# Kernel optimization log

Measured on AMD Instinct MI355X. Metric: run time of the kernel, lower is better.

The kernel has to match this reference:

```python
import jax, jax.numpy as jnp
import numpy as np

N, T, D, H = 64, 1024, 512, 512

def setup_inputs() -> dict:
    key = jax.random.key(0)
    k1, k2, k3, k4 = jax.random.split(key, 4)
    x = jax.random.normal(k1, (N, T, D), dtype=jnp.float32)
    h0 = jax.random.normal(k2, (N, H), dtype=jnp.float32)
    Wx = jax.random.normal(k3, (D, H), dtype=jnp.float32) / jnp.sqrt(jnp.float32(D))
    Wh = jax.random.normal(k4, (H, H), dtype=jnp.float32) / jnp.sqrt(jnp.float32(H))
    b = jnp.zeros((H,), dtype=jnp.float32)
    return {"x": x, "h0": h0, "Wx": Wx, "Wh": Wh, "b": b}

def reference(x, h0, Wx, Wh, b):
    # Precompute input projection for all timesteps: (N,T,H)
    xW = jnp.einsum('ntd,dh->nth', x, Wx) + b
    # Sequential recurrence over time via lax.scan
    def step(prev_h, xw_t):
        next_h = jnp.tanh(prev_h @ Wh + xw_t)  # (N,H)
        return next_h, next_h
    # scan over time axis: move T to leading axis
    _, h_seq = jax.lax.scan(step, h0, jnp.swapaxes(xW, 0, 1))  # (T,N,H)
    return jnp.swapaxes(h_seq, 0, 1)  # (N,T,H)
```

## Files before the change

kernel.cpp:

```cpp
#include <hip/hip_runtime.h>
#include <hip/hip_fp16.h>
#include <cstddef>
#include <cstdint>

#define NB 64
#define TT 1024
#define DD 512
#define HH 512

typedef _Float16 h2_t __attribute__((ext_vector_type(2)));
typedef __attribute__((ext_vector_type(8))) short bf16x8;
typedef __attribute__((ext_vector_type(4))) float f32x4;
typedef __attribute__((ext_vector_type(8))) unsigned short ushort8;

__device__ __forceinline__ float dot2f(uint32_t a, uint32_t b, float c) {
#if __has_builtin(__builtin_amdgcn_fdot2)
    return __builtin_amdgcn_fdot2(__builtin_bit_cast(h2_t, a),
                                  __builtin_bit_cast(h2_t, b), c, false);
#else
    __half2 av = __builtin_bit_cast(__half2, a);
    __half2 bv = __builtin_bit_cast(__half2, b);
    float2 af = __half22float2(av), bf = __half22float2(bv);
    return fmaf(af.x, bf.x, fmaf(af.y, bf.y, c));
#endif
}

__device__ __forceinline__ float fast_tanh(float z) {
    z = fmaxf(-15.f, fminf(15.f, z));
    float u = __builtin_amdgcn_exp2f(-2.885390082f * z);
    return (1.f - u) * __builtin_amdgcn_rcpf(1.f + u);
}

__device__ __forceinline__ unsigned short f2bf(float f) {
    uint32_t u = __builtin_bit_cast(uint32_t, f);
    u += 0x7FFFu + ((u >> 16) & 1u);
    return (unsigned short)(u >> 16);
}

__global__ void conv_x(const float* __restrict__ x,
                       unsigned short* __restrict__ xb, long total) {
    long i0 = (long)(blockIdx.x * blockDim.x + threadIdx.x) * 8;
    long stride = (long)gridDim.x * blockDim.x * 8;
    for (long i = i0; i < total; i += stride) {
        float4 a = *reinterpret_cast<const float4*>(&x[i]);
        float4 b = *reinterpret_cast<const float4*>(&x[i + 4]);
        ushort8 o;
        o[0] = f2bf(a.x); o[1] = f2bf(a.y); o[2] = f2bf(a.z); o[3] = f2bf(a.w);
        o[4] = f2bf(b.x); o[5] = f2bf(b.y); o[6] = f2bf(b.z); o[7] = f2bf(b.w);
        *reinterpret_cast<ushort8*>(&xb[i]) = o;
    }
}

__global__ void conv_wt(const float* __restrict__ W,
                        unsigned short* __restrict__ Wt) {
    int n = blockIdx.x;
    int kc = threadIdx.x;
    ushort8 o;
#pragma unroll
    for (int i = 0; i < 8; ++i)
        o[i] = f2bf(W[(size_t)(kc * 8 + i) * HH + n]);
    *reinterpret_cast<ushort8*>(&Wt[(size_t)n * DD + kc * 8]) = o;
}

#define GBM 128
#define GBN 128
#define GBK 64
#define LDSW 72

__global__ __launch_bounds__(256, 4) void gemm_bf16(
    const unsigned short* __restrict__ A,
    const unsigned short* __restrict__ Bt,
    const float* __restrict__ bias,
    float* __restrict__ C)
{
    __shared__ unsigned short As[GBM * LDSW];
    __shared__ unsigned short Bs[GBN * LDSW];

    const int tid  = threadIdx.x;
    const int m0   = blockIdx.x * GBM;
    const int n0   = blockIdx.y * GBN;
    const int lane = tid & 63;
    const int wave = tid >> 6;
    const int wm   = wave >> 1;
    const int wn   = wave & 1;

    const int srow = tid >> 3;
    const int sch  = tid & 7;

    f32x4 acc[4][4] = {};

    const int arow = wm * 64 + (lane & 15);
    const int brow = wn * 64 + (lane & 15);
    const int koff = (lane >> 4) * 8;

    for (int kt = 0; kt < DD / GBK; ++kt) {
        const int k0 = kt * GBK;
#pragma unroll
        for (int p = 0; p < 4; ++p) {
            const int row = srow + p * 32;
            *reinterpret_cast<ushort8*>(&As[row * LDSW + sch * 8]) =
                *reinterpret_cast<const ushort8*>(
                    &A[(size_t)(m0 + row) * DD + k0 + sch * 8]);
            *reinterpret_cast<ushort8*>(&Bs[row * LDSW + sch * 8]) =
                *reinterpret_cast<const ushort8*>(
                    &Bt[(size_t)(n0 + row) * DD + k0 + sch * 8]);
        }
        __syncthreads();

#pragma unroll
        for (int kk = 0; kk < GBK; kk += 32) {
            bf16x8 af[4], bf[4];
#pragma unroll
            for (int mt = 0; mt < 4; ++mt)
                af[mt] = *reinterpret_cast<const bf16x8*>(
                    &As[(arow + mt * 16) * LDSW + kk + koff]);
#pragma unroll
            for (int nt = 0; nt < 4; ++nt)
                bf[nt] = *reinterpret_cast<const bf16x8*>(
                    &Bs[(brow + nt * 16) * LDSW + kk + koff]);
#pragma unroll
            for (int mt = 0; mt < 4; ++mt)
#pragma unroll
                for (int nt = 0; nt < 4; ++nt)
                    acc[mt][nt] = __builtin_amdgcn_mfma_f32_16x16x32_bf16(
                        af[mt], bf[nt], acc[mt][nt], 0, 0, 0);
        }
        __syncthreads();
    }

#pragma unroll
    for (int nt = 0; nt < 4; ++nt) {
        const int col = n0 + wn * 64 + nt * 16 + (lane & 15);
        const float bv = bias[col];
#pragma unroll
        for (int mt = 0; mt < 4; ++mt) {
            const int rbase = m0 + wm * 64 + mt * 16 + (lane >> 4) * 4;
#pragma unroll
            for (int r = 0; r < 4; ++r)
                C[(size_t)(rbase + r) * HH + col] = acc[mt][nt][r] + bv;
        }
    }
}

#define BM 128
#define BN 128
#define BK 8

__global__ __launch_bounds__(256, 2) void gemm_xw(
    const float* __restrict__ A,
    const float* __restrict__ B,
    const float* __restrict__ bias,
    float* __restrict__ C)
{
    __shared__ float As[BK][BM];
    __shared__ float Bs[BK][BN];

    const int tid  = threadIdx.x;
    const int tm   = tid >> 4;
    const int tn   = tid & 15;
    const int row0 = blockIdx.x * BM;
    const int col0 = blockIdx.y * BN;

    const int ar = tid >> 1;
    const int ac = (tid & 1) * 4;
    const int br = tid >> 5;
    const int bc = (tid & 31) * 4;

    float acc[8][8];
#pragma unroll
    for (int i = 0; i < 8; ++i)
#pragma unroll
        for (int j = 0; j < 8; ++j) acc[i][j] = 0.f;

    for (int k0 = 0; k0 < DD; k0 += BK) {
        float4 av = *reinterpret_cast<const float4*>(
            &A[(size_t)(row0 + ar) * DD + k0 + ac]);
        float4 bv = *reinterpret_cast<const float4*>(
            &B[(size_t)(k0 + br) * HH + col0 + bc]);

        As[ac + 0][ar] = av.x;
        As[ac + 1][ar] = av.y;
        As[ac + 2][ar] = av.z;
        As[ac + 3][ar] = av.w;
        *reinterpret_cast<float4*>(&Bs[br][bc]) = bv;
        __syncthreads();

#pragma unroll
        for (int kk = 0; kk < BK; ++kk) {
            float a[8], b[8];
            *reinterpret_cast<float4*>(&a[0]) =
                *reinterpret_cast<const float4*>(&As[kk][tm * 8]);
            *reinterpret_cast<float4*>(&a[4]) =
                *reinterpret_cast<const float4*>(&As[kk][tm * 8 + 4]);
            *reinterpret_cast<float4*>(&b[0]) =
                *reinterpret_cast<const float4*>(&Bs[kk][tn * 8]);
            *reinterpret_cast<float4*>(&b[4]) =
                *reinterpret_cast<const float4*>(&Bs[kk][tn * 8 + 4]);
#pragma unroll
            for (int i = 0; i < 8; ++i)
#pragma unroll
                for (int j = 0; j < 8; ++j)
                    acc[i][j] = fmaf(a[i], b[j], acc[i][j]);
        }
        __syncthreads();
    }

#pragma unroll
    for (int i = 0; i < 8; ++i) {
        const int row = row0 + tm * 8 + i;
#pragma unroll
        for (int j = 0; j < 8; j += 4) {
            const int col = col0 + tn * 8 + j;
            float4 o;
            o.x = acc[i][j + 0] + bias[col + 0];
            o.y = acc[i][j + 1] + bias[col + 1];
            o.z = acc[i][j + 2] + bias[col + 2];
            o.w = acc[i][j + 3] + bias[col + 3];
            *reinterpret_cast<float4*>(&C[(size_t)row * HH + col]) = o;
        }
    }
}

__global__ __launch_bounds__(1024, 4) void rnn_scan_pkt(
    const float* __restrict__ Wh,
    const float* __restrict__ h0,
    float* __restrict__ out,
    uint64_t* __restrict__ exch)
{
    __shared__ __align__(16) uint32_t hp[2][HH / 2];
    __shared__ float partial[16][128];

    const int blk = blockIdx.x;
    const int x = blk & 7;
    const int i = blk >> 3;
    const int n = x + ((i & 7) << 3);
    const int r = i >> 3;
    const int jb = r << 7;

    const int tid = threadIdx.x;
    const int w = tid >> 6;
    const int l = tid & 63;

    uint32_t w0[16], w1[16];
    {
        const float* wc = Wh + (size_t)(w * 32) * HH + jb + l;
#pragma unroll
        for (int p = 0; p < 16; ++p) {
            float e0 = wc[(size_t)(2 * p) * HH];
            float e1 = wc[(size_t)(2 * p + 1) * HH];
            w0[p] = __builtin_bit_cast(uint32_t, __floats2half2_rn(e0, e1));
            float f0 = wc[(size_t)(2 * p) * HH + 64];
            float f1 = wc[(size_t)(2 * p + 1) * HH + 64];
            w1[p] = __builtin_bit_cast(uint32_t, __floats2half2_rn(f0, f1));
        }
    }

    if (tid < HH)
        ((__half*)hp[0])[tid] = __float2half(h0[(size_t)n * HH + tid]);
    __syncthreads();

    float* outn = out + (size_t)n * TT * HH;
    uint64_t* ex = exch + (size_t)n * 2 * HH;

    const int rcol = (jb + 128 + (tid - 128)) & (HH - 1);

    int cur = 0;
    for (int t = 0; t < TT; ++t) {
        const uint32_t T = (uint32_t)(t + 1);
        const int slot = (int)(T & 1u);

        float xw_r = 0.f;
        if (tid < 128) xw_r = outn[(size_t)t * HH + jb + tid];

        const uint32_t* hpw = &hp[cur][w * 16];
        float a0 = 0.f, a1 = 0.f, b0 = 0.f, b1 = 0.f;
#pragma unroll
        for (int q = 0; q < 4; ++q) {
            uint4 hv = ((const uint4*)hpw)[q];
            a0 = dot2f(hv.x, w0[4 * q + 0], a0);
            b0 = dot2f(hv.x, w1[4 * q + 0], b0);
            a1 = dot2f(hv.y, w0[4 * q + 1], a1);
            b1 = dot2f(hv.y, w1[4 * q + 1], b1);
            a0 = dot2f(hv.z, w0[4 * q + 2], a0);
            b0 = dot2f(hv.z, w1[4 * q + 2], b0);
            a1 = dot2f(hv.w, w0[4 * q + 3], a1);
            b1 = dot2f(hv.w, w1[4 * q + 3], b1);
        }
        partial[w][l] = a0 + a1;
        partial[w][64 + l] = b0 + b1;
        __syncthreads();

        __half* hpn = (__half*)hp[cur ^ 1];
        if (tid < 128) {
            float s = 0.f;
#pragma unroll
            for (int ww = 0; ww < 16; ++ww) s += partial[ww][tid];
            float h = fast_tanh(s + xw_r);
            outn[(size_t)t * HH + jb + tid] = h;
            hpn[jb + tid] = __float2half(h);
            uint64_t pk = ((uint64_t)T << 32) |
                          (uint64_t)__builtin_bit_cast(uint32_t, h);
            __hip_atomic_store(&ex[slot * HH + jb + tid], pk,
                               __ATOMIC_RELAXED, __HIP_MEMORY_SCOPE_AGENT);
        } else if (tid < 512) {
            uint64_t pk = __hip_atomic_load(&ex[slot * HH + rcol],
                                            __ATOMIC_RELAXED,
                                            __HIP_MEMORY_SCOPE_AGENT);
            while ((uint32_t)(pk >> 32) != T) {
                __builtin_amdgcn_s_sleep(1);
                pk = __hip_atomic_load(&ex[slot * HH + rcol],
                                       __ATOMIC_RELAXED,
                                       __HIP_MEMORY_SCOPE_AGENT);
            }
            hpn[rcol] = __float2half(__builtin_bit_cast(float, (uint32_t)pk));
        }
        __syncthreads();
        cur ^= 1;
    }
}

__global__ __launch_bounds__(512, 2) void rnn_scan_f32(
    const float* __restrict__ Wh,
    const float* __restrict__ h0,
    float* __restrict__ out)
{
    __shared__ float hbuf[2][HH];
    const int n = blockIdx.x;
    const int j = threadIdx.x;

    hbuf[0][j] = h0[(size_t)n * HH + j];
    __syncthreads();

    float* outn = out + (size_t)n * TT * HH;
    const float* __restrict__ wp = Wh + j;

    int cur = 0;
    for (int t = 0; t < TT; ++t) {
        float acc = outn[(size_t)t * HH + j];
        const float* hc = hbuf[cur];
#pragma unroll 4
        for (int k = 0; k < HH; k += 4) {
            float4 hv = *reinterpret_cast<const float4*>(&hc[k]);
            acc = fmaf(hv.x, wp[(size_t)(k + 0) * HH], acc);
            acc = fmaf(hv.y, wp[(size_t)(k + 1) * HH], acc);
            acc = fmaf(hv.z, wp[(size_t)(k + 2) * HH], acc);
            acc = fmaf(hv.w, wp[(size_t)(k + 3) * HH], acc);
        }
        float hn = tanhf(acc);
        outn[(size_t)t * HH + j] = hn;
        hbuf[cur ^ 1][j] = hn;
        cur ^= 1;
        __syncthreads();
    }
}

extern "C" void kernel_launch(void* const* d_in, const int* in_sizes, int n_in,
                              void* d_out, int out_size, void* d_ws, size_t ws_size,
                              hipStream_t stream) {
    const float* x  = (const float*)d_in[0];
    const float* h0 = (const float*)d_in[1];
    const float* Wx = (const float*)d_in[2];
    const float* Wh = (const float*)d_in[3];
    const float* b  = (const float*)d_in[4];
    float* out = (float*)d_out;

    const long   M        = (long)NB * TT;
    const size_t exch_b   = (size_t)NB * 2 * HH * 8;
    const size_t wt_b     = (size_t)HH * DD * 2;
    const size_t xb_b     = (size_t)M * DD * 2;
    const size_t need_mid = exch_b;
    const size_t need_all = exch_b + wt_b + xb_b;

    if (ws_size >= need_all) {
        uint64_t*       exch = (uint64_t*)d_ws;
        unsigned short* Wt   = (unsigned short*)((char*)d_ws + exch_b);
        unsigned short* xb   = (unsigned short*)((char*)d_ws + exch_b + wt_b);

        conv_x<<<2048, 256, 0, stream>>>(x, xb, M * DD);
        conv_wt<<<HH, 64, 0, stream>>>(Wx, Wt);
        dim3 gg(M / GBM, HH / GBN);
        gemm_bf16<<<gg, 256, 0, stream>>>(xb, Wt, b, out);
        rnn_scan_pkt<<<256, 1024, 0, stream>>>(Wh, h0, out, exch);
    } else if (ws_size >= need_mid) {
        dim3 g1(M / BM, HH / BN);
        gemm_xw<<<g1, 256, 0, stream>>>(x, Wx, b, out);
        rnn_scan_pkt<<<256, 1024, 0, stream>>>(Wh, h0, out, (uint64_t*)d_ws);
    } else {
        dim3 g1(M / BM, HH / BN);
        gemm_xw<<<g1, 256, 0, stream>>>(x, Wx, b, out);
        rnn_scan_f32<<<NB, 512, 0, stream>>>(Wh, h0, out);
    }
}
```

Baseline: 1.471 ms.

## Assign RNN batch groups by XCD and poll a mirror through non-coherent L2

Each block reads its hardware XCD id and claims a slot through an atomic counter. A grid-wide rendezvous then assigns the four column-slices of a batch row to blocks on the same XCD where possible. For those co-located groups, producers also write h packets to a mirror buffer, and consumers poll it with sc0 loads. This is meant to keep the per-timestep exchange in the shared L2 instead of going through device-scope coherence, with an occasional fallback check of the coherent copy. It adds a startup barrier and a memset, and relies on all 256 blocks being co-resident and on L2 visibility semantics within an XCD.

```diff
diff --git a/kernel.cpp b/kernel.cpp
--- a/kernel.cpp
+++ b/kernel.cpp
@@ -221,23 +221,62 @@
     }
 }
 
-__global__ __launch_bounds__(1024, 4) void rnn_scan_pkt(
+__global__ __launch_bounds__(1024, 4) void rnn_scan_xcd(
     const float* __restrict__ Wh,
     const float* __restrict__ h0,
     float* __restrict__ out,
-    uint64_t* __restrict__ exch)
+    uint64_t* __restrict__ truth,
+    uint64_t* __restrict__ mirror,
+    int* __restrict__ meta)
 {
     __shared__ __align__(16) uint32_t hp[2][HH / 2];
     __shared__ float partial[16][128];
-
-    const int blk = blockIdx.x;
-    const int x = blk & 7;
-    const int i = blk >> 3;
-    const int n = x + ((i & 7) << 3);
-    const int r = i >> 3;
-    const int jb = r << 7;
+    __shared__ int sh_batch, sh_role, sh_fast;
 
     const int tid = threadIdx.x;
+
+    int xcd_raw;
+    asm volatile("s_getreg_b32 %0, hwreg(HW_REG_XCC_ID)" : "=s"(xcd_raw));
+    const int xcd = xcd_raw & 7;
+
+    if (tid == 0) {
+        int pos = __hip_atomic_fetch_add(&meta[xcd], 1, __ATOMIC_RELAXED,
+                                         __HIP_MEMORY_SCOPE_AGENT);
+        __hip_atomic_fetch_add(&meta[8], 1, __ATOMIC_RELEASE,
+                               __HIP_MEMORY_SCOPE_AGENT);
+        while (__hip_atomic_load(&meta[8], __ATOMIC_ACQUIRE,
+                                 __HIP_MEMORY_SCOPE_AGENT) < 256)
+            __builtin_amdgcn_s_sleep(8);
+        int c[8];
+#pragma unroll
+        for (int q = 0; q < 8; ++q)
+            c[q] = __hip_atomic_load(&meta[q], __ATOMIC_RELAXED,
+                                     __HIP_MEMORY_SCOPE_AGENT);
+        int totalfull = 0, basefull = 0, rembase = 0;
+#pragma unroll
+        for (int q = 0; q < 8; ++q) totalfull += c[q] >> 2;
+        for (int q = 0; q < xcd; ++q) {
+            basefull += c[q] >> 2;
+            rembase  += c[q] & 3;
+        }
+        const int nf4 = (c[xcd] >> 2) << 2;
+        if (pos < nf4) {
+            sh_batch = basefull + (pos >> 2);
+            sh_role  = pos & 3;
+            sh_fast  = 1;
+        } else {
+            int ridx = rembase + (pos - nf4);
+            sh_batch = totalfull + (ridx >> 2);
+            sh_role  = ridx & 3;
+            sh_fast  = 0;
+        }
+    }
+    __syncthreads();
+
+    const int n    = sh_batch;
+    const int jb   = sh_role << 7;
+    const int fast = sh_fast;
+
     const int w = tid >> 6;
     const int l = tid & 63;
 
@@ -260,7 +299,8 @@
     __syncthreads();
 
     float* outn = out + (size_t)n * TT * HH;
-    uint64_t* ex = exch + (size_t)n * 2 * HH;
+    uint64_t* tru = truth  + (size_t)n * 2 * HH;
+    uint64_t* mir = mirror + (size_t)n * 2 * HH;
 
     const int rcol = (jb + 128 + (tid - 128)) & (HH - 1);
 
@@ -300,19 +340,40 @@
             hpn[jb + tid] = __float2half(h);
             uint64_t pk = ((uint64_t)T << 32) |
                           (uint64_t)__builtin_bit_cast(uint32_t, h);
-            __hip_atomic_store(&ex[slot * HH + jb + tid], pk,
-                               __ATOMIC_RELAXED, __HIP_MEMORY_SCOPE_AGENT);
+            const int off = slot * HH + jb + tid;
+            if (fast) {
+                asm volatile("global_store_dwordx2 %0, %1, off"
+                             :: "v"((uint64_t)&mir[off]), "v"(pk) : "memory");
+            }
+            __hip_atomic_store(&tru[off], pk, __ATOMIC_RELAXED,
+                               __HIP_MEMORY_SCOPE_AGENT);
         } else if (tid < 512) {
-            uint64_t pk = __hip_atomic_load(&ex[slot * HH + rcol],
-                                            __ATOMIC_RELAXED,
-                                            __HIP_MEMORY_SCOPE_AGENT);
-            while ((uint32_t)(pk >> 32) != T) {
-                __builtin_amdgcn_s_sleep(1);
-                pk = __hip_atomic_load(&ex[slot * HH + rcol],
-                                       __ATOMIC_RELAXED,
-                                       __HIP_MEMORY_SCOPE_AGENT);
+            const int off = slot * HH + rcol;
+            uint64_t v;
+            if (fast) {
+                uint64_t maddr = (uint64_t)&mir[off];
+                int spins = 0;
+                while (true) {
+                    asm volatile("global_load_dwordx2 %0, %1, off sc0\n\t"
+                                 "s_waitcnt vmcnt(0)"
+                                 : "=v"(v) : "v"(maddr));
+                    if ((uint32_t)(v >> 32) == T) break;
+                    if ((++spins & 7) == 0) {
+                        v = __hip_atomic_load(&tru[off], __ATOMIC_RELAXED,
+                                              __HIP_MEMORY_SCOPE_AGENT);
+                        if ((uint32_t)(v >> 32) == T) break;
+                    }
+                }
+            } else {
+                v = __hip_atomic_load(&tru[off], __ATOMIC_RELAXED,
+                                      __HIP_MEMORY_SCOPE_AGENT);
+                while ((uint32_t)(v >> 32) != T) {
+                    __builtin_amdgcn_s_sleep(1);
+                    v = __hip_atomic_load(&tru[off], __ATOMIC_RELAXED,
+                                          __HIP_MEMORY_SCOPE_AGENT);
+                }
             }
-            hpn[rcol] = __float2half(__builtin_bit_cast(float, (uint32_t)pk));
+            hpn[rcol] = __float2half(__builtin_bit_cast(float, (uint32_t)v));
         }
         __syncthreads();
         cur ^= 1;
@@ -364,27 +425,40 @@
     const float* b  = (const float*)d_in[4];
     float* out = (float*)d_out;
 
-    const long   M        = (long)NB * TT;
-    const size_t exch_b   = (size_t)NB * 2 * HH * 8;
-    const size_t wt_b     = (size_t)HH * DD * 2;
-    const size_t xb_b     = (size_t)M * DD * 2;
-    const size_t need_mid = exch_b;
-    const size_t need_all = exch_b + wt_b + xb_b;
+    const long   M      = (long)NB * TT;
+    const size_t pkt_b  = (size_t)NB * 2 * HH * 8;
+    const size_t meta_b = 4096;
+    const size_t wt_b   = (size_t)HH * DD * 2;
+    const size_t xb_b   = (size_t)M * DD * 2;
+
+    const size_t off_mir  = pkt_b;
+    const size_t off_meta = 2 * pkt_b;
+    const size_t off_wt   = 2 * pkt_b + meta_b;
+    const size_t off_xb   = off_wt + wt_b;
+    const size_t need_all = off_xb + xb_b;
+    const size_t need_mid = 2 * pkt_b + meta_b;
 
     if (ws_size >= need_all) {
-        uint64_t*       exch = (uint64_t*)d_ws;
-        unsigned short* Wt   = (unsigned short*)((char*)d_ws + exch_b);
-        unsigned short* xb   = (unsigned short*)((char*)d_ws + exch_b + wt_b);
-
+        uint64_t*       truth  = (uint64_t*)d_ws;
+        uint64_t*       mirror = (uint64_t*)((char*)d_ws + off_mir);
+        int*            meta   = (int*)((char*)d_ws + off_meta);
+        unsigned short* Wt     = (unsigned short*)((char*)d_ws + off_wt);
+        unsigned short* xb     = (unsigned short*)((char*)d_ws + off_xb);
+
+        hipMemsetAsync(meta, 0, 64, stream);
         conv_x<<<2048, 256, 0, stream>>>(x, xb, M * DD);
         conv_wt<<<HH, 64, 0, stream>>>(Wx, Wt);
         dim3 gg(M / GBM, HH / GBN);
         gemm_bf16<<<gg, 256, 0, stream>>>(xb, Wt, b, out);
-        rnn_scan_pkt<<<256, 1024, 0, stream>>>(Wh, h0, out, exch);
+        rnn_scan_xcd<<<256, 1024, 0, stream>>>(Wh, h0, out, truth, mirror, meta);
     } else if (ws_size >= need_mid) {
+        uint64_t* truth  = (uint64_t*)d_ws;
+        uint64_t* mirror = (uint64_t*)((char*)d_ws + off_mir);
+        int*      meta   = (int*)((char*)d_ws + off_meta);
+        hipMemsetAsync(meta, 0, 64, stream);
         dim3 g1(M / BM, HH / BN);
         gemm_xw<<<g1, 256, 0, stream>>>(x, Wx, b, out);
-        rnn_scan_pkt<<<256, 1024, 0, stream>>>(Wh, h0, out, (uint64_t*)d_ws);
+        rnn_scan_xcd<<<256, 1024, 0, stream>>>(Wh, h0, out, truth, mirror, meta);
     } else {
         dim3 g1(M / BM, HH / BN);
         gemm_xw<<<g1, 256, 0, stream>>>(x, Wx, b, out);
```

Result: slower. 2.356 ms (+60.2%).

## Pack two batch sequences per scan block, halving grid size

Applied to the files above, without the earlier changes.

The recurrent scan kernel now handles two batch rows per 1024-thread block: each 512-thread half owns one sequence and holds twice as many Wh rows in registers (64 half2 per thread). The grid drops from 256 to 128 blocks, so the Wh slice is loaded once per block and shared across two sequences, and fewer blocks take part in the cross-block exchange. In exchange, each wave does twice the dot-product work per step, register pressure rises, and the per-step critical path within a block gets longer.

```diff
diff --git a/kernel.cpp b/kernel.cpp
--- a/kernel.cpp
+++ b/kernel.cpp
@@ -221,31 +221,33 @@
     }
 }
 
-__global__ __launch_bounds__(1024, 4) void rnn_scan_pkt(
+__global__ __launch_bounds__(1024, 4) void rnn_scan_dual(
     const float* __restrict__ Wh,
     const float* __restrict__ h0,
     float* __restrict__ out,
     uint64_t* __restrict__ exch)
 {
-    __shared__ __align__(16) uint32_t hp[2][HH / 2];
-    __shared__ float partial[16][128];
-
-    const int blk = blockIdx.x;
-    const int x = blk & 7;
-    const int i = blk >> 3;
-    const int n = x + ((i & 7) << 3);
-    const int r = i >> 3;
-    const int jb = r << 7;
-
-    const int tid = threadIdx.x;
-    const int w = tid >> 6;
-    const int l = tid & 63;
-
-    uint32_t w0[16], w1[16];
+    __shared__ __align__(16) uint32_t hp[2][2][HH / 2];
+    __shared__ float partial[2][8][128];
+
+    const int b   = blockIdx.x;
+    const int g   = b & 31;
+    const int r   = b >> 5;
+    const int jb  = r << 7;
+
+    const int tid   = threadIdx.x;
+    const int s     = tid >> 9;
+    const int local = tid & 511;
+    const int n     = 2 * g + s;
+
+    const int w = local >> 6;
+    const int l = local & 63;
+
+    uint32_t w0[32], w1[32];
     {
-        const float* wc = Wh + (size_t)(w * 32) * HH + jb + l;
-#pragma unroll
-        for (int p = 0; p < 16; ++p) {
+        const float* wc = Wh + (size_t)(w * 64) * HH + jb + l;
+#pragma unroll
+        for (int p = 0; p < 32; ++p) {
             float e0 = wc[(size_t)(2 * p) * HH];
             float e1 = wc[(size_t)(2 * p + 1) * HH];
             w0[p] = __builtin_bit_cast(uint32_t, __floats2half2_rn(e0, e1));
@@ -255,14 +257,13 @@
         }
     }
 
-    if (tid < HH)
-        ((__half*)hp[0])[tid] = __float2half(h0[(size_t)n * HH + tid]);
+    ((__half*)hp[s][0])[local] = __float2half(h0[(size_t)n * HH + local]);
     __syncthreads();
 
     float* outn = out + (size_t)n * TT * HH;
     uint64_t* ex = exch + (size_t)n * 2 * HH;
 
-    const int rcol = (jb + 128 + (tid - 128)) & (HH - 1);
+    const int rcol = (jb + 128 + (local - 128)) & (HH - 1);
 
     int cur = 0;
     for (int t = 0; t < TT; ++t) {
@@ -270,12 +271,12 @@
         const int slot = (int)(T & 1u);
 
         float xw_r = 0.f;
-        if (tid < 128) xw_r = outn[(size_t)t * HH + jb + tid];
-
-        const uint32_t* hpw = &hp[cur][w * 16];
+        if (local < 128) xw_r = outn[(size_t)t * HH + jb + local];
+
+        const uint32_t* hpw = &hp[s][cur][w * 32];
         float a0 = 0.f, a1 = 0.f, b0 = 0.f, b1 = 0.f;
 #pragma unroll
-        for (int q = 0; q < 4; ++q) {
+        for (int q = 0; q < 8; ++q) {
             uint4 hv = ((const uint4*)hpw)[q];
             a0 = dot2f(hv.x, w0[4 * q + 0], a0);
             b0 = dot2f(hv.x, w1[4 * q + 0], b0);
@@ -286,23 +287,23 @@
             a1 = dot2f(hv.w, w0[4 * q + 3], a1);
             b1 = dot2f(hv.w, w1[4 * q + 3], b1);
         }
-        partial[w][l] = a0 + a1;
-        partial[w][64 + l] = b0 + b1;
-        __syncthreads();
-
-        __half* hpn = (__half*)hp[cur ^ 1];
-        if (tid < 128) {
-            float s = 0.f;
-#pragma unroll
-            for (int ww = 0; ww < 16; ++ww) s += partial[ww][tid];
-            float h = fast_tanh(s + xw_r);
-            outn[(size_t)t * HH + jb + tid] = h;
-            hpn[jb + tid] = __float2half(h);
+        partial[s][w][l] = a0 + a1;
+        partial[s][w][64 + l] = b0 + b1;
+        __syncthreads();
+
+        __half* hpn = (__half*)hp[s][cur ^ 1];
+        if (local < 128) {
+            float sum = 0.f;
+#pragma unroll
+            for (int ww = 0; ww < 8; ++ww) sum += partial[s][ww][local];
+            float h = fast_tanh(sum + xw_r);
+            outn[(size_t)t * HH + jb + local] = h;
+            hpn[jb + local] = __float2half(h);
             uint64_t pk = ((uint64_t)T << 32) |
                           (uint64_t)__builtin_bit_cast(uint32_t, h);
-            __hip_atomic_store(&ex[slot * HH + jb + tid], pk,
+            __hip_atomic_store(&ex[slot * HH + jb + local], pk,
                                __ATOMIC_RELAXED, __HIP_MEMORY_SCOPE_AGENT);
-        } else if (tid < 512) {
+        } else {
             uint64_t pk = __hip_atomic_load(&ex[slot * HH + rcol],
                                             __ATOMIC_RELAXED,
                                             __HIP_MEMORY_SCOPE_AGENT);
@@ -364,12 +365,12 @@
     const float* b  = (const float*)d_in[4];
     float* out = (float*)d_out;
 
-    const long   M        = (long)NB * TT;
-    const size_t exch_b   = (size_t)NB * 2 * HH * 8;
-    const size_t wt_b     = (size_t)HH * DD * 2;
-    const size_t xb_b     = (size_t)M * DD * 2;
+    const long   M      = (long)NB * TT;
+    const size_t exch_b = (size_t)NB * 2 * HH * 8;
+    const size_t wt_b   = (size_t)HH * DD * 2;
+    const size_t xb_b   = (size_t)M * DD * 2;
+    const size_t need_all = exch_b + wt_b + xb_b;
     const size_t need_mid = exch_b;
-    const size_t need_all = exch_b + wt_b + xb_b;
 
     if (ws_size >= need_all) {
         uint64_t*       exch = (uint64_t*)d_ws;
@@ -380,11 +381,11 @@
         conv_wt<<<HH, 64, 0, stream>>>(Wx, Wt);
         dim3 gg(M / GBM, HH / GBN);
         gemm_bf16<<<gg, 256, 0, stream>>>(xb, Wt, b, out);
-        rnn_scan_pkt<<<256, 1024, 0, stream>>>(Wh, h0, out, exch);
+        rnn_scan_dual<<<128, 1024, 0, stream>>>(Wh, h0, out, exch);
     } else if (ws_size >= need_mid) {
         dim3 g1(M / BM, HH / BN);
         gemm_xw<<<g1, 256, 0, stream>>>(x, Wx, b, out);
-        rnn_scan_pkt<<<256, 1024, 0, stream>>>(Wh, h0, out, (uint64_t*)d_ws);
+        rnn_scan_dual<<<128, 1024, 0, stream>>>(Wh, h0, out, (uint64_t*)d_ws);
     } else {
         dim3 g1(M / BM, HH / BN);
         gemm_xw<<<g1, 256, 0, stream>>>(x, Wx, b, out);
```

Result: slower. 1.736 ms (+18.0%).
